# Performance work log

Measured on AMD Instinct MI355X. Metric: run time of the kernel, lower is better.

The kernel has to match this reference:

```python
import jax, jax.numpy as jnp
import numpy as np

N_NODES = 100000
N_EDGES = 1600000
IN_DIM, HID_DIM, OUT_DIM = 2, 128, 128


def setup_inputs() -> dict:
    key = jax.random.key(0)
    ks = jax.random.split(key, 8)
    x = jax.random.normal(ks[0], (N_NODES, IN_DIM), dtype=jnp.float32)
    edge_index = jax.random.randint(ks[1], (2, N_EDGES), 0, N_NODES, dtype=jnp.int64)
    s = 0.1
    return {
        "x": x,
        "edge_index": edge_index,
        # SAGEConv layer 1: lin_l (on aggregated neighbors, with bias) + lin_r (root)
        "W_l1": jax.random.normal(ks[2], (IN_DIM, HID_DIM), dtype=jnp.float32) * s,
        "W_r1": jax.random.normal(ks[3], (IN_DIM, HID_DIM), dtype=jnp.float32) * s,
        "b1": jnp.zeros((HID_DIM,), dtype=jnp.float32),
        # SAGEConv layer 2
        "W_l2": jax.random.normal(ks[4], (HID_DIM, OUT_DIM), dtype=jnp.float32) * s,
        "W_r2": jax.random.normal(ks[5], (HID_DIM, OUT_DIM), dtype=jnp.float32) * s,
        "b2": jnp.zeros((OUT_DIM,), dtype=jnp.float32),
    }


def _sage_conv(h, src, dst, Wl, Wr, b):
    # PyG SAGEConv (aggr='mean'): out_i = Wl @ mean_{j in N(i)} h_j + Wr @ h_i + b
    msg = h[src]                                              # [E, D] gather
    agg = jax.ops.segment_sum(msg, dst, num_segments=N_NODES)  # [N, D] scatter-add
    deg = jax.ops.segment_sum(jnp.ones_like(dst, dtype=h.dtype), dst,
                              num_segments=N_NODES)
    agg = agg / jnp.maximum(deg, 1.0)[:, None]                # mean aggregation
    return agg @ Wl + h @ Wr + b


def reference(x, edge_index, W_l1, W_r1, b1, W_l2, W_r2, b2):
    src, dst = edge_index[0], edge_index[1]  # messages flow src -> dst
    h = _sage_conv(x, src, dst, W_l1, W_r1, b1)
    h = jax.nn.relu(h)  # dropout p=0.1 is identity in eval mode
    out = _sage_conv(h, src, dst, W_l2, W_r2, b2)
    return out
```

## Files before the change

kernel.cpp:

```cpp
#include <hip/hip_runtime.h>


using f32x4 = __attribute__((ext_vector_type(4))) float;
using f32x2 = __attribute__((ext_vector_type(2))) float;
using s16x8 = __attribute__((ext_vector_type(8))) short;

__device__ __forceinline__ unsigned short f32_to_bf16(float f) {
  unsigned int u = __float_as_uint(f);
  u += 0x7fffu + ((u >> 16) & 1u);
  return (unsigned short)(u >> 16);
}

#define EDGE_TILE 4096
#define NBMAX 1600

__global__ __launch_bounds__(256) void k_bhist(const int* __restrict__ ei, int* __restrict__ bcnt,
                                               unsigned short* __restrict__ hcnt, int E, int nb) {
  __shared__ int h[NBMAX];
  int t = threadIdx.x;
  for (int i = t; i < nb; i += 256) h[i] = 0;
  __syncthreads();
  int tbeg = blockIdx.x * EDGE_TILE;
  int tend = min(tbeg + EDGE_TILE, E);
  const int* dstp = ei + E;
  for (int i = tbeg + t; i < tend; i += 256) atomicAdd(&h[dstp[i] >> 6], 1);
  __syncthreads();
  unsigned short* hr = hcnt + (size_t)blockIdx.x * nb;
  for (int i = t; i < nb; i += 256) {
    int c = h[i];
    hr[i] = (unsigned short)c;
    if (c) atomicAdd(&bcnt[i], c);
  }
}

__global__ __launch_bounds__(256) void k_scans(const unsigned short* __restrict__ hcnt,
                                               unsigned short* __restrict__ rel,
                                               const int* __restrict__ bcnt,
                                               int* __restrict__ bbase,
                                               const float* __restrict__ Wl2,
                                               const float* __restrict__ Wr2,
                                               unsigned short* __restrict__ wt,
                                               int nblk, int nb, int E) {
  __shared__ int sm[2][256];
  int bb = blockIdx.x;
  int t = threadIdx.x;

  if (bb < nb) {
    int b = bb;
    int e0 = 2 * t, e1 = 2 * t + 1;
    int a = (e0 < nblk) ? (int)hcnt[(size_t)e0 * nb + b] : 0;
    int c = (e1 < nblk) ? (int)hcnt[(size_t)e1 * nb + b] : 0;
    int s = a + c;
    sm[0][t] = s;
    __syncthreads();
    int src = 0;
    for (int st = 1; st < 256; st <<= 1) {
      int v = sm[src][t];
      if (t >= st) v += sm[src][t - st];
      sm[src ^ 1][t] = v; __syncthreads(); src ^= 1;
    }
    int excl = sm[src][t] - s;
    if (e0 < nblk) rel[(size_t)e0 * nb + b] = (unsigned short)excl;
    if (e1 < nblk) rel[(size_t)e1 * nb + b] = (unsigned short)(excl + a);
  } else if (bb == nb) {
    int i0 = t * 8;
    int v[8];
    int s = 0;
#pragma unroll
    for (int j = 0; j < 8; ++j) {
      v[j] = (i0 + j < nb) ? bcnt[i0 + j] : 0;
      s += v[j];
    }
    sm[0][t] = s;
    __syncthreads();
    int src = 0;
    for (int st = 1; st < 256; st <<= 1) {
      int vv = sm[src][t];
      if (t >= st) vv += sm[src][t - st];
      sm[src ^ 1][t] = vv; __syncthreads(); src ^= 1;
    }
    int ex = sm[src][t] - s;
#pragma unroll
    for (int j = 0; j < 8; ++j) {
      if (i0 + j < nb) bbase[i0 + j] = ex;
      ex += v[j];
    }
    if (t == 255) bbase[nb] = E;
  } else {
    int tid = (bb - nb - 1) * 256 + t;
    if (tid < 128 * 256) {
      int c = tid >> 8, k = tid & 255;
      float v = (k < 128) ? Wl2[k * 128 + c] : Wr2[(k - 128) * 128 + c];
      wt[tid] = f32_to_bf16(v);
    }
  }
}

__global__ __launch_bounds__(256) void k_bscatter(const int* __restrict__ ei,
                                                  const int* __restrict__ bbase,
                                                  const unsigned short* __restrict__ rel,
                                                  unsigned int* __restrict__ ebuf, int E, int nb) {
  __shared__ int h[NBMAX];
  __shared__ int base[NBMAX];
  int t = threadIdx.x;
  const unsigned short* rr = rel + (size_t)blockIdx.x * nb;
  for (int i = t; i < nb; i += 256) {
    h[i] = 0;
    base[i] = bbase[i] + (int)rr[i];
  }
  __syncthreads();
  int tbeg = blockIdx.x * EDGE_TILE;
  int tend = min(tbeg + EDGE_TILE, E);
  const int* srcp = ei;
  const int* dstp = ei + E;
  for (int i = tbeg + t; i < tend; i += 256) {
    int d = dstp[i];
    int b = d >> 6;
    int r = atomicAdd(&h[b], 1);
    ebuf[base[b] + r] = ((unsigned)srcp[i] << 6) | (unsigned)(d & 63);
  }
}

__global__ __launch_bounds__(256) void k_bucket_csr(const unsigned int* __restrict__ ebuf,
                                                    const int* __restrict__ bbase,
                                                    const float* __restrict__ x,
                                                    const float* __restrict__ Wl,
                                                    const float* __restrict__ Wr,
                                                    const float* __restrict__ b1,
                                                    int* __restrict__ offs, int* __restrict__ csr,
                                                    unsigned int* __restrict__ h16,
                                                    unsigned short* __restrict__ h8,
                                                    int N, int nb) {
  __shared__ int deg[64];
  __shared__ int loff[64];
  __shared__ int exo[64];
  __shared__ int cur[64];
  __shared__ float sx0[64];
  __shared__ float sx1[64];
  int b = blockIdx.x;
  int t = threadIdx.x;
  int lo = bbase[b], hi = bbase[b + 1];
  if (t < 64) deg[t] = 0;
  __syncthreads();

  for (int i = lo + t; i < hi; i += 256) atomicAdd(&deg[ebuf[i] & 63], 1);
  __syncthreads();

  if (t < 64) loff[t] = deg[t];
  __syncthreads();
  for (int st = 1; st < 64; st <<= 1) {
    int v = 0;
    if (t < 64 && t >= st) v = loff[t - st];
    __syncthreads();
    if (t < 64) loff[t] += v;
    __syncthreads();
  }
  if (t < 64) {
    int ex = loff[t] - deg[t];
    exo[t] = ex;
    cur[t] = ex;
    int node = b * 64 + t;
    if (node < N) offs[node] = lo + ex;
  }
  if (b == nb - 1 && t == 0) offs[N] = hi;
  __syncthreads();

  for (int i = lo + t; i < hi; i += 256) {
    unsigned int e = ebuf[i];
    int r = atomicAdd(&cur[e & 63], 1);
    csr[lo + r] = (int)(e >> 6);
  }
  __syncthreads();

  const float2* x2 = (const float2*)x;
  {
    int nl = t >> 2;
    int node = b * 64 + nl;
    float ax = 0.f, ay = 0.f;
    if (node < N) {
      int base = lo + exo[nl];
      int dg = deg[nl];
      for (int j = (t & 3); j < dg; j += 4) {
        float2 v = x2[csr[base + j]];
        ax += v.x;
        ay += v.y;
      }
    }
    ax += __shfl_xor(ax, 1);
    ay += __shfl_xor(ay, 1);
    ax += __shfl_xor(ax, 2);
    ay += __shfl_xor(ay, 2);
    if ((t & 3) == 0) { sx0[nl] = ax; sx1[nl] = ay; }
  }
  __syncthreads();

  int nfirst = b * 64;
  for (int i = t; i < 64 * 64; i += 256) {
    int nl = i >> 6;
    int node = nfirst + nl;
    if (node >= N) break;
    int c = (i & 63) * 2;
    int dg = deg[nl];
    float sc = 1.0f / (float)max(dg, 1);
    float a0 = sx0[nl] * sc, a1 = sx1[nl] * sc;
    float2 xv = x2[node];
    float r0 = fmaf(a0, Wl[c],     fmaf(a1, Wl[128 + c],     fmaf(xv.x, Wr[c],     fmaf(xv.y, Wr[128 + c],     b1[c]))));
    float r1 = fmaf(a0, Wl[c + 1], fmaf(a1, Wl[128 + c + 1], fmaf(xv.x, Wr[c + 1], fmaf(xv.y, Wr[128 + c + 1], b1[c + 1]))));
    r0 = r0 > 0.f ? r0 : 0.f;
    r1 = r1 > 0.f ? r1 : 0.f;
    unsigned int packed = (unsigned int)f32_to_bf16(r0) | ((unsigned int)f32_to_bf16(r1) << 16);
    h16[(size_t)node * 64 + (i & 63)] = packed;
    unsigned int p8 = (unsigned int)__builtin_amdgcn_cvt_pk_fp8_f32(r0, r1, 0, false);
    h8[(size_t)node * 64 + (i & 63)] = (unsigned short)(p8 & 0xffffu);
  }
}

#define ACC8(v)                                                                              \
  do {                                                                                       \
    f32x2 p;                                                                                 \
    p = __builtin_amdgcn_cvt_pk_f32_fp8((int)(v).x, false); acc[0] += p[0];  acc[1] += p[1]; \
    p = __builtin_amdgcn_cvt_pk_f32_fp8((int)(v).x, true);  acc[2] += p[0];  acc[3] += p[1]; \
    p = __builtin_amdgcn_cvt_pk_f32_fp8((int)(v).y, false); acc[4] += p[0];  acc[5] += p[1]; \
    p = __builtin_amdgcn_cvt_pk_f32_fp8((int)(v).y, true);  acc[6] += p[0];  acc[7] += p[1]; \
    p = __builtin_amdgcn_cvt_pk_f32_fp8((int)(v).z, false); acc[8] += p[0];  acc[9] += p[1]; \
    p = __builtin_amdgcn_cvt_pk_f32_fp8((int)(v).z, true);  acc[10] += p[0]; acc[11] += p[1];\
    p = __builtin_amdgcn_cvt_pk_f32_fp8((int)(v).w, false); acc[12] += p[0]; acc[13] += p[1];\
    p = __builtin_amdgcn_cvt_pk_f32_fp8((int)(v).w, true);  acc[14] += p[0]; acc[15] += p[1];\
  } while (0)

__global__ __launch_bounds__(256) void k_agg2(const int* __restrict__ offs, const int* __restrict__ csr,
                                              const unsigned char* __restrict__ h8,
                                              unsigned int* __restrict__ a16, int n) {
  int wv   = threadIdx.x >> 6;
  int lane = threadIdx.x & 63;
  int sub  = lane >> 3;
  int cb   = lane & 7;
  int node = blockIdx.x * 32 + wv * 8 + sub;
  if (node >= n) return;
  int beg = offs[node];
  int end = offs[node + 1];
  int deg = end - beg;
  const unsigned char* hb = h8 + cb * 16;

  float acc[16];
#pragma unroll
  for (int j = 0; j < 16; ++j) acc[j] = 0.f;

  int t = 0;
  if (deg >= 2) {
    int s0 = csr[beg];
    int s1 = csr[beg + 1];
    uint4 c0 = *(const uint4*)(hb + (size_t)s0 * 128);
    uint4 c1 = *(const uint4*)(hb + (size_t)s1 * 128);
    for (t = 2; t + 1 < deg; t += 2) {
      int n0 = csr[beg + t];
      int n1 = csr[beg + t + 1];
      uint4 p0 = *(const uint4*)(hb + (size_t)n0 * 128);
      uint4 p1 = *(const uint4*)(hb + (size_t)n1 * 128);
      ACC8(c0);
      ACC8(c1);
      c0 = p0; c1 = p1;
    }
    ACC8(c0);
    ACC8(c1);
  }
  if (t < deg) {
    int s0 = csr[beg + t];
    uint4 v0 = *(const uint4*)(hb + (size_t)s0 * 128);
    ACC8(v0);
  }

  float scale = 1.0f / (float)max(deg, 1);
  unsigned int u[8];
#pragma unroll
  for (int k = 0; k < 8; ++k)
    u[k] = (unsigned int)f32_to_bf16(acc[2 * k] * scale) |
           ((unsigned int)f32_to_bf16(acc[2 * k + 1] * scale) << 16);
  unsigned int* dst = a16 + (size_t)node * 64 + cb * 8;
  *(uint4*)dst       = make_uint4(u[0], u[1], u[2], u[3]);
  *(uint4*)(dst + 4) = make_uint4(u[4], u[5], u[6], u[7]);
}

__global__ __launch_bounds__(256) void k_gemm(const unsigned short* __restrict__ a16,
                                              const unsigned short* __restrict__ h16,
                                              const unsigned short* __restrict__ wt,
                                              const float* __restrict__ b2,
                                              float* __restrict__ out, int nrows) {
  __shared__ unsigned short bs[64 * 264];
  int half = blockIdx.x & 1;
  int tg   = blockIdx.x >> 1;

#pragma unroll
  for (int i = 0; i < 8; ++i) {
    int c = threadIdx.x + i * 256;
    int row = c >> 5, off = c & 31;
    *(uint4*)(bs + row * 264 + off * 8) =
        *(const uint4*)(wt + ((size_t)(half * 64 + row)) * 256 + off * 8);
  }
  __syncthreads();

  int wv   = threadIdx.x >> 6;
  int lane = threadIdx.x & 63;
  int m16 = lane & 15, quad = lane >> 4;
  int tile = tg * 4 + wv;
  if (tile * 16 >= nrows) return;

  int r  = tile * 16 + m16;
  int rc = r < nrows ? r : nrows - 1;
  const unsigned short* arow = a16 + (size_t)rc * 128 + quad * 8;
  const unsigned short* hrow = h16 + (size_t)rc * 128 + quad * 8;

  s16x8 afrag[8];
#pragma unroll
  for (int c4 = 0; c4 < 4; ++c4) {
    afrag[c4]     = *(const s16x8*)(arow + c4 * 32);
    afrag[4 + c4] = *(const s16x8*)(hrow + c4 * 32);
  }

  f32x4 acc[4];
#pragma unroll
  for (int t = 0; t < 4; ++t) acc[t] = (f32x4){0.f, 0.f, 0.f, 0.f};

  const unsigned short* bbase = bs + m16 * 264 + quad * 8;
#pragma unroll
  for (int ch = 0; ch < 8; ++ch) {
#pragma unroll
    for (int t = 0; t < 4; ++t) {
      s16x8 bf = *(const s16x8*)(bbase + t * 16 * 264 + ch * 32);
      acc[t] = __builtin_amdgcn_mfma_f32_16x16x32_bf16(afrag[ch], bf, acc[t], 0, 0, 0);
    }
  }

#pragma unroll
  for (int t = 0; t < 4; ++t) {
    int col = half * 64 + t * 16 + m16;
    float bias = b2[col];
#pragma unroll
    for (int i = 0; i < 4; ++i) {
      int row = tile * 16 + quad * 4 + i;
      if (row < nrows) out[(size_t)row * 128 + col] = acc[t][i] + bias;
    }
  }
}

extern "C" void kernel_launch(void* const* d_in, const int* in_sizes, int n_in,
                              void* d_out, int out_size, void* d_ws, size_t ws_size,
                              hipStream_t stream) {
  const float* x    = (const float*)d_in[0];
  const int*   ei   = (const int*)d_in[1];
  const float* Wl1  = (const float*)d_in[2];
  const float* Wr1  = (const float*)d_in[3];
  const float* b1   = (const float*)d_in[4];
  const float* Wl2  = (const float*)d_in[5];
  const float* Wr2  = (const float*)d_in[6];
  const float* b2   = (const float*)d_in[7];
  float* out = (float*)d_out;

  const int N = in_sizes[0] / 2;
  const int E = in_sizes[1] / 2;
  const int nb = (N + 63) >> 6;
  const int nblk_e = (E + EDGE_TILE - 1) / EDGE_TILE;

  char* p = (char*)d_ws;
  auto take = [&](size_t bytes) { char* r = p; p += (bytes + 255) & ~(size_t)255; return r; };
  int* bcnt            = (int*)take((size_t)NBMAX * 4);
  int* bbase           = (int*)take((size_t)(NBMAX + 1) * 4);
  unsigned short* hcnt = (unsigned short*)take((size_t)nblk_e * nb * 2);
  unsigned short* rel  = (unsigned short*)take((size_t)nblk_e * nb * 2);
  int* offs            = (int*)take((size_t)(N + 1) * 4);
  int* csr             = (int*)take((size_t)E * 4);
  unsigned int* ebuf   = (unsigned int*)take((size_t)E * 4);
  unsigned short* h16  = (unsigned short*)take((size_t)N * 128 * 2);
  unsigned short* a16  = (unsigned short*)take((size_t)N * 128 * 2);
  unsigned short* h8   = (unsigned short*)take((size_t)N * 128);
  unsigned short* wt   = (unsigned short*)take((size_t)128 * 256 * 2);

  const int ntiles = (N + 15) / 16;

  hipMemsetAsync(bcnt, 0, (size_t)NBMAX * 4, stream);

  k_bhist     <<<nblk_e, 256, 0, stream>>>(ei, bcnt, hcnt, E, nb);
  k_scans     <<<nb + 1 + 128, 256, 0, stream>>>(hcnt, rel, bcnt, bbase, Wl2, Wr2, wt,
                                                 nblk_e, nb, E);
  k_bscatter  <<<nblk_e, 256, 0, stream>>>(ei, bbase, rel, ebuf, E, nb);
  k_bucket_csr<<<nb, 256, 0, stream>>>(ebuf, bbase, x, Wl1, Wr1, b1, offs, csr,
                                       (unsigned int*)h16, h8, N, nb);
  k_agg2      <<<(N + 31) / 32, 256, 0, stream>>>(offs, csr, (const unsigned char*)h8,
                                                  (unsigned int*)a16, N);
  k_gemm      <<<((ntiles + 3) / 4) * 2, 256, 0, stream>>>(a16, h16, wt, b2, out, N);
}
```

Measured before the change: 239.7 us.

## Split fp8 features into per-XCD column slices for L2-resident gather

The fp8 hidden features are stored as 8 column slices of 16 bytes per node instead of row-major 128-byte rows. The aggregation kernel now assigns one thread per node per slice, with the slice chosen by blockIdx&7. If blocks are dispatched round-robin across the 8 XCDs, each XCD gathers only one ~1.6MB slice, which can stay resident in its L2. The aggregated output and the GEMM's A-operand loads are moved to the same slice-major layout. In exchange, each CSR neighbour list is read 8 times, and each gather is a scattered 16-byte access rather than a coalesced 128-byte row.

```diff
diff --git a/kernel.cpp b/kernel.cpp
--- a/kernel.cpp
+++ b/kernel.cpp
@@ -199,7 +199,8 @@
     int nl = i >> 6;
     int node = nfirst + nl;
     if (node >= N) break;
-    int c = (i & 63) * 2;
+    int cp = i & 63;
+    int c = cp * 2;
     int dg = deg[nl];
     float sc = 1.0f / (float)max(dg, 1);
     float a0 = sx0[nl] * sc, a1 = sx1[nl] * sc;
@@ -209,9 +210,9 @@
     r0 = r0 > 0.f ? r0 : 0.f;
     r1 = r1 > 0.f ? r1 : 0.f;
     unsigned int packed = (unsigned int)f32_to_bf16(r0) | ((unsigned int)f32_to_bf16(r1) << 16);
-    h16[(size_t)node * 64 + (i & 63)] = packed;
+    h16[(size_t)node * 64 + cp] = packed;
     unsigned int p8 = (unsigned int)__builtin_amdgcn_cvt_pk_fp8_f32(r0, r1, 0, false);
-    h8[(size_t)node * 64 + (i & 63)] = (unsigned short)(p8 & 0xffffu);
+    h8[(size_t)(cp >> 3) * N * 8 + (size_t)node * 8 + (cp & 7)] = (unsigned short)(p8 & 0xffffu);
   }
 }
 
@@ -231,16 +232,14 @@
 __global__ __launch_bounds__(256) void k_agg2(const int* __restrict__ offs, const int* __restrict__ csr,
                                               const unsigned char* __restrict__ h8,
                                               unsigned int* __restrict__ a16, int n) {
-  int wv   = threadIdx.x >> 6;
-  int lane = threadIdx.x & 63;
-  int sub  = lane >> 3;
-  int cb   = lane & 7;
-  int node = blockIdx.x * 32 + wv * 8 + sub;
+  int slice = blockIdx.x & 7;
+  int chunk = blockIdx.x >> 3;
+  int node  = chunk * 256 + threadIdx.x;
   if (node >= n) return;
   int beg = offs[node];
   int end = offs[node + 1];
   int deg = end - beg;
-  const unsigned char* hb = h8 + cb * 16;
+  const unsigned char* hs = h8 + (size_t)slice * n * 16;
 
   float acc[16];
 #pragma unroll
@@ -250,13 +249,13 @@
   if (deg >= 2) {
     int s0 = csr[beg];
     int s1 = csr[beg + 1];
-    uint4 c0 = *(const uint4*)(hb + (size_t)s0 * 128);
-    uint4 c1 = *(const uint4*)(hb + (size_t)s1 * 128);
+    uint4 c0 = *(const uint4*)(hs + (size_t)s0 * 16);
+    uint4 c1 = *(const uint4*)(hs + (size_t)s1 * 16);
     for (t = 2; t + 1 < deg; t += 2) {
       int n0 = csr[beg + t];
       int n1 = csr[beg + t + 1];
-      uint4 p0 = *(const uint4*)(hb + (size_t)n0 * 128);
-      uint4 p1 = *(const uint4*)(hb + (size_t)n1 * 128);
+      uint4 p0 = *(const uint4*)(hs + (size_t)n0 * 16);
+      uint4 p1 = *(const uint4*)(hs + (size_t)n1 * 16);
       ACC8(c0);
       ACC8(c1);
       c0 = p0; c1 = p1;
@@ -266,7 +265,7 @@
   }
   if (t < deg) {
     int s0 = csr[beg + t];
-    uint4 v0 = *(const uint4*)(hb + (size_t)s0 * 128);
+    uint4 v0 = *(const uint4*)(hs + (size_t)s0 * 16);
     ACC8(v0);
   }
 
@@ -276,7 +275,7 @@
   for (int k = 0; k < 8; ++k)
     u[k] = (unsigned int)f32_to_bf16(acc[2 * k] * scale) |
            ((unsigned int)f32_to_bf16(acc[2 * k + 1] * scale) << 16);
-  unsigned int* dst = a16 + (size_t)node * 64 + cb * 8;
+  unsigned int* dst = a16 + (size_t)slice * n * 8 + (size_t)node * 8;
   *(uint4*)dst       = make_uint4(u[0], u[1], u[2], u[3]);
   *(uint4*)(dst + 4) = make_uint4(u[4], u[5], u[6], u[7]);
 }
@@ -307,13 +306,15 @@
 
   int r  = tile * 16 + m16;
   int rc = r < nrows ? r : nrows - 1;
-  const unsigned short* arow = a16 + (size_t)rc * 128 + quad * 8;
   const unsigned short* hrow = h16 + (size_t)rc * 128 + quad * 8;
 
   s16x8 afrag[8];
 #pragma unroll
   for (int c4 = 0; c4 < 4; ++c4) {
-    afrag[c4]     = *(const s16x8*)(arow + c4 * 32);
+    int col0 = c4 * 32 + quad * 8;
+    const unsigned short* ap = a16 + (size_t)(col0 >> 4) * nrows * 16
+                                   + (size_t)rc * 16 + (col0 & 15);
+    afrag[c4]     = *(const s16x8*)ap;
     afrag[4 + c4] = *(const s16x8*)(hrow + c4 * 32);
   }
 
@@ -376,6 +377,7 @@
   unsigned short* wt   = (unsigned short*)take((size_t)128 * 256 * 2);
 
   const int ntiles = (N + 15) / 16;
+  const int nch    = (N + 255) / 256;
 
   hipMemsetAsync(bcnt, 0, (size_t)NBMAX * 4, stream);
 
@@ -385,7 +387,7 @@
   k_bscatter  <<<nblk_e, 256, 0, stream>>>(ei, bbase, rel, ebuf, E, nb);
   k_bucket_csr<<<nb, 256, 0, stream>>>(ebuf, bbase, x, Wl1, Wr1, b1, offs, csr,
                                        (unsigned int*)h16, h8, N, nb);
-  k_agg2      <<<(N + 31) / 32, 256, 0, stream>>>(offs, csr, (const unsigned char*)h8,
-                                                  (unsigned int*)a16, N);
+  k_agg2      <<<nch * 8, 256, 0, stream>>>(offs, csr, (const unsigned char*)h8,
+                                            (unsigned int*)a16, N);
   k_gemm      <<<((ntiles + 3) / 4) * 2, 256, 0, stream>>>(a16, h16, wt, b2, out, N);
 }
```

Result: slower. 281.9 us (+17.6%).

## Split layer-1 compute out of CSR build into wave-per-node kernel

Applied to the files above, without the earlier changes.

Moves the layer-1 neighbor mean and 2->128 linear+ReLU out of the bucket CSR kernel into a separate kernel with one wavefront per node. The CSR kernel becomes lighter, and layer 1 gets far more parallelism (100k waves instead of 1563 blocks). The cost is an extra kernel launch, re-reading offs/csr from global memory, and wasting most lanes for low-degree nodes (average degree 16 on 64 lanes).

```diff
diff --git a/kernel.cpp b/kernel.cpp
--- a/kernel.cpp
+++ b/kernel.cpp
@@ -123,20 +123,11 @@
 
 __global__ __launch_bounds__(256) void k_bucket_csr(const unsigned int* __restrict__ ebuf,
                                                     const int* __restrict__ bbase,
-                                                    const float* __restrict__ x,
-                                                    const float* __restrict__ Wl,
-                                                    const float* __restrict__ Wr,
-                                                    const float* __restrict__ b1,
                                                     int* __restrict__ offs, int* __restrict__ csr,
-                                                    unsigned int* __restrict__ h16,
-                                                    unsigned short* __restrict__ h8,
                                                     int N, int nb) {
   __shared__ int deg[64];
   __shared__ int loff[64];
-  __shared__ int exo[64];
   __shared__ int cur[64];
-  __shared__ float sx0[64];
-  __shared__ float sx1[64];
   int b = blockIdx.x;
   int t = threadIdx.x;
   int lo = bbase[b], hi = bbase[b + 1];
@@ -157,7 +148,6 @@
   }
   if (t < 64) {
     int ex = loff[t] - deg[t];
-    exo[t] = ex;
     cur[t] = ex;
     int node = b * 64 + t;
     if (node < N) offs[node] = lo + ex;
@@ -170,49 +160,49 @@
     int r = atomicAdd(&cur[e & 63], 1);
     csr[lo + r] = (int)(e >> 6);
   }
-  __syncthreads();
-
+}
+
+__global__ __launch_bounds__(256) void k_layer1(const float* __restrict__ x,
+                                                const int* __restrict__ offs,
+                                                const int* __restrict__ csr,
+                                                const float* __restrict__ Wl,
+                                                const float* __restrict__ Wr,
+                                                const float* __restrict__ b1,
+                                                unsigned int* __restrict__ h16,
+                                                unsigned short* __restrict__ h8, int n) {
+  int wv = threadIdx.x >> 6;
+  int lane = threadIdx.x & 63;
+  int node = blockIdx.x * 4 + wv;
+  if (node >= n) return;
+  int beg = offs[node];
+  int end = offs[node + 1];
+  int deg = end - beg;
   const float2* x2 = (const float2*)x;
-  {
-    int nl = t >> 2;
-    int node = b * 64 + nl;
-    float ax = 0.f, ay = 0.f;
-    if (node < N) {
-      int base = lo + exo[nl];
-      int dg = deg[nl];
-      for (int j = (t & 3); j < dg; j += 4) {
-        float2 v = x2[csr[base + j]];
-        ax += v.x;
-        ay += v.y;
-      }
-    }
-    ax += __shfl_xor(ax, 1);
-    ay += __shfl_xor(ay, 1);
-    ax += __shfl_xor(ax, 2);
-    ay += __shfl_xor(ay, 2);
-    if ((t & 3) == 0) { sx0[nl] = ax; sx1[nl] = ay; }
-  }
-  __syncthreads();
-
-  int nfirst = b * 64;
-  for (int i = t; i < 64 * 64; i += 256) {
-    int nl = i >> 6;
-    int node = nfirst + nl;
-    if (node >= N) break;
-    int c = (i & 63) * 2;
-    int dg = deg[nl];
-    float sc = 1.0f / (float)max(dg, 1);
-    float a0 = sx0[nl] * sc, a1 = sx1[nl] * sc;
-    float2 xv = x2[node];
-    float r0 = fmaf(a0, Wl[c],     fmaf(a1, Wl[128 + c],     fmaf(xv.x, Wr[c],     fmaf(xv.y, Wr[128 + c],     b1[c]))));
-    float r1 = fmaf(a0, Wl[c + 1], fmaf(a1, Wl[128 + c + 1], fmaf(xv.x, Wr[c + 1], fmaf(xv.y, Wr[128 + c + 1], b1[c + 1]))));
-    r0 = r0 > 0.f ? r0 : 0.f;
-    r1 = r1 > 0.f ? r1 : 0.f;
-    unsigned int packed = (unsigned int)f32_to_bf16(r0) | ((unsigned int)f32_to_bf16(r1) << 16);
-    h16[(size_t)node * 64 + (i & 63)] = packed;
-    unsigned int p8 = (unsigned int)__builtin_amdgcn_cvt_pk_fp8_f32(r0, r1, 0, false);
-    h8[(size_t)node * 64 + (i & 63)] = (unsigned short)(p8 & 0xffffu);
-  }
+
+  float ax = 0.f, ay = 0.f;
+  for (int t = lane; t < deg; t += 64) {
+    float2 v = x2[csr[beg + t]];
+    ax += v.x;
+    ay += v.y;
+  }
+#pragma unroll
+  for (int off = 32; off; off >>= 1) {
+    ax += __shfl_xor(ax, off);
+    ay += __shfl_xor(ay, off);
+  }
+  float sc = 1.0f / (float)max(deg, 1);
+  float a0 = ax * sc, a1 = ay * sc;
+  float2 xv = x2[node];
+
+  int c = lane * 2;
+  float r0 = fmaf(a0, Wl[c],     fmaf(a1, Wl[128 + c],     fmaf(xv.x, Wr[c],     fmaf(xv.y, Wr[128 + c],     b1[c]))));
+  float r1 = fmaf(a0, Wl[c + 1], fmaf(a1, Wl[128 + c + 1], fmaf(xv.x, Wr[c + 1], fmaf(xv.y, Wr[128 + c + 1], b1[c + 1]))));
+  r0 = r0 > 0.f ? r0 : 0.f;
+  r1 = r1 > 0.f ? r1 : 0.f;
+  unsigned int packed = (unsigned int)f32_to_bf16(r0) | ((unsigned int)f32_to_bf16(r1) << 16);
+  h16[(size_t)node * 64 + lane] = packed;
+  unsigned int p8 = (unsigned int)__builtin_amdgcn_cvt_pk_fp8_f32(r0, r1, 0, false);
+  h8[(size_t)node * 64 + lane] = (unsigned short)(p8 & 0xffffu);
 }
 
 #define ACC8(v)                                                                              \
@@ -383,8 +373,9 @@
   k_scans     <<<nb + 1 + 128, 256, 0, stream>>>(hcnt, rel, bcnt, bbase, Wl2, Wr2, wt,
                                                  nblk_e, nb, E);
   k_bscatter  <<<nblk_e, 256, 0, stream>>>(ei, bbase, rel, ebuf, E, nb);
-  k_bucket_csr<<<nb, 256, 0, stream>>>(ebuf, bbase, x, Wl1, Wr1, b1, offs, csr,
-                                       (unsigned int*)h16, h8, N, nb);
+  k_bucket_csr<<<nb, 256, 0, stream>>>(ebuf, bbase, offs, csr, N, nb);
+  k_layer1    <<<(N + 3) / 4, 256, 0, stream>>>(x, offs, csr, Wl1, Wr1, b1,
+                                                (unsigned int*)h16, h8, N);
   k_agg2      <<<(N + 31) / 32, 256, 0, stream>>>(offs, csr, (const unsigned char*)h8,
                                                   (unsigned int*)a16, N);
   k_gemm      <<<((ntiles + 3) / 4) * 2, 256, 0, stream>>>(a16, h16, wt, b2, out, N);
```

New measurement: 239.4 us. No clear change (-0.1%).
